# Kernel tuning notes

Hardware: AMD Instinct MI355X
Metric: run time of the kernel (lower is better)

Reference implementation:

```python
import jax, jax.numpy as jnp
import numpy as np


def setup_inputs() -> dict:
    key = jax.random.key(0)
    ks = jax.random.split(key, 8)
    B, IN, H, OUT = 8192, 1024, 2048, 1024
    SIGMA_MIN, SIGMA_MAX, PHASE = 0.9, 0.999, 2.0 * np.pi
    # recurrence decay params, initialized as in the torch module
    rng = np.random.RandomState(0)
    u1 = rng.random_sample(H)
    u2 = rng.random_sample(H)
    v = -0.5 * np.log(u1 * (SIGMA_MAX ** 2 - SIGMA_MIN ** 2) + SIGMA_MIN ** 2)
    theta = u2 * PHASE
    scale_b = 1.0 / np.sqrt(IN)
    scale_c = 1.0 / np.sqrt(H)
    return {
        "x": jax.random.normal(ks[0], (B, IN), dtype=jnp.float32),
        "h_prev": jax.random.normal(ks[1], (B, H), dtype=jnp.float32),
        "Br": jax.random.normal(ks[2], (H, IN), dtype=jnp.float32) * scale_b,
        "Bi": jax.random.normal(ks[3], (H, IN), dtype=jnp.float32) * scale_b,
        "Cr": jax.random.normal(ks[4], (OUT, H), dtype=jnp.float32) * scale_c,
        "Ci": jax.random.normal(ks[5], (OUT, H), dtype=jnp.float32) * scale_c,
        "v_log": jnp.asarray(np.log(v), dtype=jnp.float32),
        "theta_log": jnp.asarray(np.log(theta), dtype=jnp.float32),
    }


def reference(x, h_prev, Br, Bi, Cr, Ci, v_log, theta_log):
    # effective diagonal recurrence weight w = exp(-exp(v_log) + i*exp(theta_log))
    mag = jnp.exp(-jnp.exp(v_log))            # [H]
    ang = jnp.exp(theta_log)                  # [H]
    wr = mag * jnp.cos(ang)
    wi = mag * jnp.sin(ang)
    # h = B(x) + h_prev * w  (h_prev is real -> imag part comes only from wi)
    # complexLinear on real x: real = x@Br^T, imag = x@Bi^T
    hr = jnp.einsum('bi,hi->bh', x, Br) + h_prev * wr   # [B,H]
    hi = jnp.einsum('bi,hi->bh', x, Bi) + h_prev * wi   # [B,H]
    # out = Re(C(h)) = hr@Cr^T - hi@Ci^T
    out = jnp.einsum('bh,oh->bo', hr, Cr) - jnp.einsum('bh,oh->bo', hi, Ci)
    return out
```

## Files before the change

kernel.cpp:

```cpp
#include <hip/hip_runtime.h>
#include <stdint.h>

typedef unsigned short u16;
typedef short bf16x8 __attribute__((ext_vector_type(8)));
typedef float f32x4 __attribute__((ext_vector_type(4)));

typedef void as1_void __attribute__((address_space(1)));
typedef void as3_void __attribute__((address_space(3)));

__device__ inline u16 f32_to_bf16(float f) {
    uint32_t u = __builtin_bit_cast(uint32_t, f);
    u += 0x7fffu + ((u >> 16) & 1u);
    return (u16)(u >> 16);
}

__device__ inline void gld_lds16(const void* g, void* l) {
    __builtin_amdgcn_global_load_lds((as1_void*)g, (as3_void*)l, 16, 0, 0);
}



__global__ void prep_w_kernel(const float* __restrict__ v_log,
                              const float* __restrict__ theta_log,
                              float* __restrict__ wfull, int H) {
    int h = blockIdx.x * blockDim.x + threadIdx.x;
    if (h < H) {
        float mag = expf(-expf(v_log[h]));
        float ang = expf(theta_log[h]);
        wfull[h]     = mag * cosf(ang);
        wfull[h + H] = mag * sinf(ang);
    }
}

__global__ void pack_ccat_kernel(const float* __restrict__ Cr,
                                 const float* __restrict__ Ci,
                                 u16* __restrict__ Ccat, int total4) {
    int i = blockIdx.x * blockDim.x + threadIdx.x;
    if (i >= total4) return;
    int e = i * 4;
    int o = e >> 12;
    int k = e & 4095;
    float4 f; float s;
    if (k < 2048) { f = *(const float4*)(Cr + (size_t)o * 2048 + k);          s =  1.f; }
    else          { f = *(const float4*)(Ci + (size_t)o * 2048 + (k - 2048)); s = -1.f; }
    ushort4 u;
    u.x = f32_to_bf16(s * f.x); u.y = f32_to_bf16(s * f.y);
    u.z = f32_to_bf16(s * f.z); u.w = f32_to_bf16(s * f.w);
    ((ushort4*)Ccat)[i] = u;
}

__global__ void transpose_cast_kernel(const float* __restrict__ Br,
                                      const float* __restrict__ Bi,
                                      u16* __restrict__ Bcat) {
    __shared__ float t[32][33];
    const float* src = blockIdx.z ? Bi : Br;
    int colOff = blockIdx.z ? 2048 : 0;
    int c0 = blockIdx.x * 32, r0 = blockIdx.y * 32;
    int tx = threadIdx.x, ty = threadIdx.y;
#pragma unroll
    for (int j = 0; j < 4; j++)
        t[ty + j * 8][tx] = src[(size_t)(r0 + ty + j * 8) * 1024 + c0 + tx];
    __syncthreads();
#pragma unroll
    for (int j = 0; j < 4; j++)
        Bcat[(size_t)(c0 + ty + j * 8) * 4096 + colOff + r0 + tx] =
            f32_to_bf16(t[tx][ty + j * 8]);
}

__global__ void cast_both_kernel(const float* __restrict__ x,
                                 const float* __restrict__ h_prev,
                                 u16* __restrict__ dst) {
    const int n4x = 8192 * 1024 / 4;
    int i = blockIdx.x * blockDim.x + threadIdx.x;
    float4 f = (i < n4x) ? ((const float4*)x)[i] : ((const float4*)h_prev)[i - n4x];
    ushort4 o;
    o.x = f32_to_bf16(f.x); o.y = f32_to_bf16(f.y);
    o.z = f32_to_bf16(f.z); o.w = f32_to_bf16(f.w);
    ((ushort4*)dst)[i] = o;
}

__global__ void reduce_cw_kernel(const float* __restrict__ partials,
                                 const float* __restrict__ Cr, const float* __restrict__ Ci,
                                 const float* __restrict__ wfull,
                                 u16* __restrict__ Wmain, u16* __restrict__ Cwbf) {
    const int n4_red = 1024 * 1024 / 4;
    const int n4_cw  = 1024 * 2048 / 4;
    int i = blockIdx.x * blockDim.x + threadIdx.x;
    if (i < n4_red) {
        int e = i * 4;
        float4 s = *(const float4*)(partials + e);
#pragma unroll
        for (int z = 1; z < 8; z++) {
            float4 p = *(const float4*)(partials + ((size_t)z << 20) + e);
            s.x += p.x; s.y += p.y; s.z += p.z; s.w += p.w;
        }
        ushort4 u;
        u.x = f32_to_bf16(s.x); u.y = f32_to_bf16(s.y);
        u.z = f32_to_bf16(s.z); u.w = f32_to_bf16(s.w);
        ((ushort4*)Wmain)[i] = u;
    } else if (i < n4_red + n4_cw) {
        int j = i - n4_red;
        int e = j * 4;
        int o = e >> 11;
        int h = e & 2047;
        float4 cr = *(const float4*)(Cr + (size_t)o * 2048 + h);
        float4 ci = *(const float4*)(Ci + (size_t)o * 2048 + h);
        float4 wr = *(const float4*)(wfull + h);
        float4 wi = *(const float4*)(wfull + 2048 + h);
        ushort4 u;
        u.x = f32_to_bf16(cr.x * wr.x - ci.x * wi.x);
        u.y = f32_to_bf16(cr.y * wr.y - ci.y * wi.y);
        u.z = f32_to_bf16(cr.z * wr.z - ci.z * wi.z);
        u.w = f32_to_bf16(cr.w * wr.w - ci.w * wi.w);
        ((ushort4*)Cwbf)[j] = u;
    }
}


__global__ __launch_bounds__(256)
void gemm_splitk_kernel(const u16* __restrict__ A, const u16* __restrict__ B,
                        float* __restrict__ partials)
{
    __shared__ __align__(16) u16 ldsA[128 * 64];
    __shared__ __align__(16) u16 ldsB[128 * 64];
    const int K = 4096;

    const int tid = threadIdx.x, wid = tid >> 6, lane = tid & 63;
    const int quad = lane >> 4, l16 = lane & 15;
    const int wm = wid >> 1, wn = wid & 1;
    const int bm = blockIdx.y, bn = blockIdx.x, bz = blockIdx.z;
    const int kb = bz * 512;

    const u16* gA[4]; const u16* gB[4];
    u16 *lA[4], *lB[4];
#pragma unroll
    for (int t = 0; t < 4; t++) {
        int s = wid * 256 + t * 64 + lane;
        int sr = s >> 3;
        int sj = (s & 7) ^ (sr & 7);
        lA[t] = ldsA + s * 8;
        lB[t] = ldsB + s * 8;
        gA[t] = A + (size_t)(bm * 128 + sr) * K + sj * 8 + kb;
        gB[t] = B + (size_t)(bn * 128 + sr) * K + sj * 8 + kb;
    }

    const f32x4 fz = {0.f, 0.f, 0.f, 0.f};
    f32x4 acc[4][4];
#pragma unroll
    for (int i = 0; i < 4; i++)
#pragma unroll
        for (int j = 0; j < 4; j++) acc[i][j] = fz;

    for (int k0 = 0; k0 < 512; k0 += 64) {
        __syncthreads();
#pragma unroll
        for (int t = 0; t < 4; t++) {
            gld_lds16(gA[t] + k0, lA[t]);
            gld_lds16(gB[t] + k0, lB[t]);
        }
        __syncthreads();
#pragma unroll
        for (int ks = 0; ks < 2; ks++) {
            bf16x8 af[4], bfr[4];
#pragma unroll
            for (int i = 0; i < 4; i++) {
                int r = wm * 64 + i * 16 + l16;
                af[i] = *(const bf16x8*)(ldsA + (r * 8 + ((ks * 4 + quad) ^ (r & 7))) * 8);
            }
#pragma unroll
            for (int j = 0; j < 4; j++) {
                int r = wn * 64 + j * 16 + l16;
                bfr[j] = *(const bf16x8*)(ldsB + (r * 8 + ((ks * 4 + quad) ^ (r & 7))) * 8);
            }
#pragma unroll
            for (int i = 0; i < 4; i++)
#pragma unroll
                for (int j = 0; j < 4; j++)
                    acc[i][j] = __builtin_amdgcn_mfma_f32_16x16x32_bf16(af[i], bfr[j], acc[i][j], 0, 0, 0);
        }
    }

    float* P = partials + ((size_t)bz << 20);
    const int gm = bm * 128 + wm * 64, gn = bn * 128 + wn * 64;
#pragma unroll
    for (int i = 0; i < 4; i++)
#pragma unroll
        for (int j = 0; j < 4; j++) {
            int col = gn + j * 16 + l16;
#pragma unroll
            for (int r = 0; r < 4; r++)
                P[(size_t)(gm + i * 16 + quad * 4 + r) * 1024 + col] = acc[i][j][r];
        }
}


__global__ __launch_bounds__(256)
void gemm_main_kernel(const u16* __restrict__ Axb, const u16* __restrict__ Ahb,
                      const u16* __restrict__ Bw,  const u16* __restrict__ Bcw,
                      float* __restrict__ out)
{
    __shared__ __align__(16) u16 ldsA[128 * 64];
    __shared__ __align__(16) u16 ldsB[128 * 64];

    const int tid = threadIdx.x, wid = tid >> 6, lane = tid & 63;
    const int quad = lane >> 4, l16 = lane & 15;
    const int wm = wid >> 1, wn = wid & 1;
    const int id = blockIdx.x;
    const int bm = id & 63, bn = id >> 6;

    int srow[4], sj[4];
    u16 *lA[4], *lB[4];
#pragma unroll
    for (int t = 0; t < 4; t++) {
        int s = wid * 256 + t * 64 + lane;
        srow[t] = s >> 3;
        sj[t] = (s & 7) ^ (srow[t] & 7);
        lA[t] = ldsA + s * 8;
        lB[t] = ldsB + s * 8;
    }

    const f32x4 fz = {0.f, 0.f, 0.f, 0.f};
    f32x4 acc[4][4];
#pragma unroll
    for (int i = 0; i < 4; i++)
#pragma unroll
        for (int j = 0; j < 4; j++) acc[i][j] = fz;

#pragma unroll 1
    for (int phase = 0; phase < 2; phase++) {
        const u16* Ap = phase ? Ahb : Axb;
        const u16* Bp = phase ? Bcw : Bw;
        const int KS = phase ? 2048 : 1024;
        const u16* gA[4]; const u16* gB[4];
#pragma unroll
        for (int t = 0; t < 4; t++) {
            gA[t] = Ap + (size_t)(bm * 128 + srow[t]) * KS + sj[t] * 8;
            gB[t] = Bp + (size_t)(bn * 128 + srow[t]) * KS + sj[t] * 8;
        }
        for (int k0 = 0; k0 < KS; k0 += 64) {
            __syncthreads();
#pragma unroll
            for (int t = 0; t < 4; t++) {
                gld_lds16(gA[t] + k0, lA[t]);
                gld_lds16(gB[t] + k0, lB[t]);
            }
            __syncthreads();
#pragma unroll
            for (int ks = 0; ks < 2; ks++) {
                bf16x8 af[4], bfr[4];
#pragma unroll
                for (int i = 0; i < 4; i++) {
                    int r = wm * 64 + i * 16 + l16;
                    af[i] = *(const bf16x8*)(ldsA + (r * 8 + ((ks * 4 + quad) ^ (r & 7))) * 8);
                }
#pragma unroll
                for (int j = 0; j < 4; j++) {
                    int r = wn * 64 + j * 16 + l16;
                    bfr[j] = *(const bf16x8*)(ldsB + (r * 8 + ((ks * 4 + quad) ^ (r & 7))) * 8);
                }
#pragma unroll
                for (int i = 0; i < 4; i++)
#pragma unroll
                    for (int j = 0; j < 4; j++)
                        acc[i][j] = __builtin_amdgcn_mfma_f32_16x16x32_bf16(af[i], bfr[j], acc[i][j], 0, 0, 0);
            }
        }
    }

    const int gm = bm * 128 + wm * 64, gn = bn * 128 + wn * 64;
#pragma unroll
    for (int i = 0; i < 4; i++)
#pragma unroll
        for (int j = 0; j < 4; j++) {
            int col = gn + j * 16 + l16;
#pragma unroll
            for (int r = 0; r < 4; r++)
                out[(size_t)(gm + i * 16 + quad * 4 + r) * 1024 + col] = acc[i][j][r];
        }
}


extern "C" void kernel_launch(void* const* d_in, const int* in_sizes, int n_in,
                              void* d_out, int out_size, void* d_ws, size_t ws_size,
                              hipStream_t stream)
{
    const float* x      = (const float*)d_in[0];
    const float* h_prev = (const float*)d_in[1];
    const float* Br     = (const float*)d_in[2];
    const float* Bi     = (const float*)d_in[3];
    const float* Cr     = (const float*)d_in[4];
    const float* Ci     = (const float*)d_in[5];
    const float* v_log  = (const float*)d_in[6];
    const float* th_log = (const float*)d_in[7];
    float* out = (float*)d_out;

    const size_t MB = 1024 * 1024;
    size_t need = 54 * MB + 4096 * 4;
    if (ws_size < need) return;

    char* ws = (char*)d_ws;
    u16*   Ccat     = (u16*)ws;
    u16*   Bcat     = (u16*)(ws + 8 * MB);
    float* partials = (float*)(ws + 16 * MB);
    u16*   x_bf     = (u16*)ws;
    u16*   hp_bf    = (u16*)(ws + 16 * MB);
    u16*   Wmain    = (u16*)(ws + 48 * MB);
    u16*   Cwbf     = (u16*)(ws + 50 * MB);
    float* wfull    = (float*)(ws + 54 * MB);

    prep_w_kernel<<<8, 256, 0, stream>>>(v_log, th_log, wfull, 2048);
    pack_ccat_kernel<<<4096, 256, 0, stream>>>(Cr, Ci, Ccat, 1024 * 4096 / 4);
    transpose_cast_kernel<<<dim3(32, 64, 2), dim3(32, 8), 0, stream>>>(Br, Bi, Bcat);
    gemm_splitk_kernel<<<dim3(8, 8, 8), 256, 0, stream>>>(Ccat, Bcat, partials);
    reduce_cw_kernel<<<3072, 256, 0, stream>>>(partials, Cr, Ci, wfull, Wmain, Cwbf);
    cast_both_kernel<<<24576, 256, 0, stream>>>(x, h_prev, x_bf);
    gemm_main_kernel<<<512, 256, 0, stream>>>(x_bf, hp_bf, Wmain, Cwbf, out);
}
```

Baseline: 250.9 us.

## Fuse prep kernels: merge casts, inline C packing into split-K GEMM, inline w

Merges the x/h_prev cast and the Br/Bi transpose-cast into one launch, removes the separate Ccat packing kernel by having the split-K GEMM load fp32 Cr/Ci and convert them to bf16 (with sign flip) on the fly into LDS, and computes the recurrence weights inline in the reduce kernel instead of a prep kernel. This cuts three kernel launches and one intermediate bf16 buffer round-trip. In exchange, the GEMM A-path now uses register loads instead of async global-to-LDS loads, and the transcendental work is repeated per output row in the reduce kernel. The workspace layout also grows.

Measured after the change: 258.8 us. +3.1%, slower.

```diff
diff --git a/kernel.cpp b/kernel.cpp
--- a/kernel.cpp
+++ b/kernel.cpp
@@ -20,68 +20,44 @@
 
 
 
-__global__ void prep_w_kernel(const float* __restrict__ v_log,
-                              const float* __restrict__ theta_log,
-                              float* __restrict__ wfull, int H) {
-    int h = blockIdx.x * blockDim.x + threadIdx.x;
-    if (h < H) {
-        float mag = expf(-expf(v_log[h]));
-        float ang = expf(theta_log[h]);
-        wfull[h]     = mag * cosf(ang);
-        wfull[h + H] = mag * sinf(ang);
-    }
-}
-
-__global__ void pack_ccat_kernel(const float* __restrict__ Cr,
-                                 const float* __restrict__ Ci,
-                                 u16* __restrict__ Ccat, int total4) {
-    int i = blockIdx.x * blockDim.x + threadIdx.x;
-    if (i >= total4) return;
-    int e = i * 4;
-    int o = e >> 12;
-    int k = e & 4095;
-    float4 f; float s;
-    if (k < 2048) { f = *(const float4*)(Cr + (size_t)o * 2048 + k);          s =  1.f; }
-    else          { f = *(const float4*)(Ci + (size_t)o * 2048 + (k - 2048)); s = -1.f; }
-    ushort4 u;
-    u.x = f32_to_bf16(s * f.x); u.y = f32_to_bf16(s * f.y);
-    u.z = f32_to_bf16(s * f.z); u.w = f32_to_bf16(s * f.w);
-    ((ushort4*)Ccat)[i] = u;
-}
-
-__global__ void transpose_cast_kernel(const float* __restrict__ Br,
-                                      const float* __restrict__ Bi,
-                                      u16* __restrict__ Bcat) {
-    __shared__ float t[32][33];
-    const float* src = blockIdx.z ? Bi : Br;
-    int colOff = blockIdx.z ? 2048 : 0;
-    int c0 = blockIdx.x * 32, r0 = blockIdx.y * 32;
-    int tx = threadIdx.x, ty = threadIdx.y;
-#pragma unroll
-    for (int j = 0; j < 4; j++)
-        t[ty + j * 8][tx] = src[(size_t)(r0 + ty + j * 8) * 1024 + c0 + tx];
-    __syncthreads();
-#pragma unroll
-    for (int j = 0; j < 4; j++)
-        Bcat[(size_t)(c0 + ty + j * 8) * 4096 + colOff + r0 + tx] =
-            f32_to_bf16(t[tx][ty + j * 8]);
-}
-
-__global__ void cast_both_kernel(const float* __restrict__ x,
-                                 const float* __restrict__ h_prev,
-                                 u16* __restrict__ dst) {
+__global__ void bigcast_kernel(const float* __restrict__ x,
+                               const float* __restrict__ h_prev,
+                               const float* __restrict__ Br,
+                               const float* __restrict__ Bi,
+                               u16* __restrict__ xh_bf,
+                               u16* __restrict__ Bcat) {
     const int n4x = 8192 * 1024 / 4;
-    int i = blockIdx.x * blockDim.x + threadIdx.x;
-    float4 f = (i < n4x) ? ((const float4*)x)[i] : ((const float4*)h_prev)[i - n4x];
-    ushort4 o;
-    o.x = f32_to_bf16(f.x); o.y = f32_to_bf16(f.y);
-    o.z = f32_to_bf16(f.z); o.w = f32_to_bf16(f.w);
-    ((ushort4*)dst)[i] = o;
-}
+    const int tid = threadIdx.x;
+    if (blockIdx.x < 24576) {
+        int i = blockIdx.x * 256 + tid;
+        float4 f = (i < n4x) ? ((const float4*)x)[i] : ((const float4*)h_prev)[i - n4x];
+        ushort4 o;
+        o.x = f32_to_bf16(f.x); o.y = f32_to_bf16(f.y);
+        o.z = f32_to_bf16(f.z); o.w = f32_to_bf16(f.w);
+        ((ushort4*)xh_bf)[i] = o;
+    } else {
+        __shared__ float t[32][33];
+        int id2 = blockIdx.x - 24576;
+        const float* src = (id2 >= 2048) ? Bi : Br;
+        int colOff = (id2 >= 2048) ? 2048 : 0;
+        int rem = id2 & 2047;
+        int c0 = (rem & 31) * 32, r0 = (rem >> 5) * 32;
+        int tx = tid & 31, ty = tid >> 5;
+#pragma unroll
+        for (int j = 0; j < 4; j++)
+            t[ty + j * 8][tx] = src[(size_t)(r0 + ty + j * 8) * 1024 + c0 + tx];
+        __syncthreads();
+#pragma unroll
+        for (int j = 0; j < 4; j++)
+            Bcat[(size_t)(c0 + ty + j * 8) * 4096 + colOff + r0 + tx] =
+                f32_to_bf16(t[tx][ty + j * 8]);
+    }
+}
+
 
 __global__ void reduce_cw_kernel(const float* __restrict__ partials,
                                  const float* __restrict__ Cr, const float* __restrict__ Ci,
-                                 const float* __restrict__ wfull,
+                                 const float* __restrict__ v_log, const float* __restrict__ th_log,
                                  u16* __restrict__ Wmain, u16* __restrict__ Cwbf) {
     const int n4_red = 1024 * 1024 / 4;
     const int n4_cw  = 1024 * 2048 / 4;
@@ -105,43 +81,52 @@
         int h = e & 2047;
         float4 cr = *(const float4*)(Cr + (size_t)o * 2048 + h);
         float4 ci = *(const float4*)(Ci + (size_t)o * 2048 + h);
-        float4 wr = *(const float4*)(wfull + h);
-        float4 wi = *(const float4*)(wfull + 2048 + h);
+        float4 vl = *(const float4*)(v_log + h);
+        float4 tl = *(const float4*)(th_log + h);
+        float mag, ang;
         ushort4 u;
-        u.x = f32_to_bf16(cr.x * wr.x - ci.x * wi.x);
-        u.y = f32_to_bf16(cr.y * wr.y - ci.y * wi.y);
-        u.z = f32_to_bf16(cr.z * wr.z - ci.z * wi.z);
-        u.w = f32_to_bf16(cr.w * wr.w - ci.w * wi.w);
+        mag = expf(-expf(vl.x)); ang = expf(tl.x);
+        u.x = f32_to_bf16(cr.x * (mag * cosf(ang)) - ci.x * (mag * sinf(ang)));
+        mag = expf(-expf(vl.y)); ang = expf(tl.y);
+        u.y = f32_to_bf16(cr.y * (mag * cosf(ang)) - ci.y * (mag * sinf(ang)));
+        mag = expf(-expf(vl.z)); ang = expf(tl.z);
+        u.z = f32_to_bf16(cr.z * (mag * cosf(ang)) - ci.z * (mag * sinf(ang)));
+        mag = expf(-expf(vl.w)); ang = expf(tl.w);
+        u.w = f32_to_bf16(cr.w * (mag * cosf(ang)) - ci.w * (mag * sinf(ang)));
         ((ushort4*)Cwbf)[j] = u;
     }
 }
 
 
 __global__ __launch_bounds__(256)
-void gemm_splitk_kernel(const u16* __restrict__ A, const u16* __restrict__ B,
-                        float* __restrict__ partials)
+void gemm_splitk_kernel(const float* __restrict__ Cr, const float* __restrict__ Ci,
+                        const u16* __restrict__ Bcat, float* __restrict__ partials)
 {
     __shared__ __align__(16) u16 ldsA[128 * 64];
     __shared__ __align__(16) u16 ldsB[128 * 64];
-    const int K = 4096;
 
     const int tid = threadIdx.x, wid = tid >> 6, lane = tid & 63;
     const int quad = lane >> 4, l16 = lane & 15;
     const int wm = wid >> 1, wn = wid & 1;
     const int bm = blockIdx.y, bn = blockIdx.x, bz = blockIdx.z;
-    const int kb = bz * 512;
-
-    const u16* gA[4]; const u16* gB[4];
-    u16 *lA[4], *lB[4];
+
+    const float* Asrc = (bz < 4) ? Cr : Ci;
+    const uint32_t sgn_mask = (bz < 4) ? 0u : 0x80000000u;
+    const int akb = (bz < 4) ? bz * 512 : bz * 512 - 2048;
+
+    const int ar = tid >> 1;
+    const int ac = (tid & 1) * 32;
+    const float* agp = Asrc + (size_t)(bm * 128 + ar) * 2048 + akb + ac;
+
+    const u16* gB[4];
+    u16* lB[4];
 #pragma unroll
     for (int t = 0; t < 4; t++) {
         int s = wid * 256 + t * 64 + lane;
         int sr = s >> 3;
         int sj = (s & 7) ^ (sr & 7);
-        lA[t] = ldsA + s * 8;
         lB[t] = ldsB + s * 8;
-        gA[t] = A + (size_t)(bm * 128 + sr) * K + sj * 8 + kb;
-        gB[t] = B + (size_t)(bn * 128 + sr) * K + sj * 8 + kb;
+        gB[t] = Bcat + (size_t)(bn * 128 + sr) * 4096 + sj * 8 + bz * 512;
     }
 
     const f32x4 fz = {0.f, 0.f, 0.f, 0.f};
@@ -154,9 +139,26 @@
     for (int k0 = 0; k0 < 512; k0 += 64) {
         __syncthreads();
 #pragma unroll
-        for (int t = 0; t < 4; t++) {
-            gld_lds16(gA[t] + k0, lA[t]);
+        for (int t = 0; t < 4; t++)
             gld_lds16(gB[t] + k0, lB[t]);
+        float4 av[8];
+#pragma unroll
+        for (int q = 0; q < 8; q++)
+            av[q] = *(const float4*)(agp + k0 + q * 4);
+#pragma unroll
+        for (int c = 0; c < 4; c++) {
+            bf16x8 w;
+            const float4 a0 = av[2 * c], a1 = av[2 * c + 1];
+            w[0] = (short)f32_to_bf16(__builtin_bit_cast(float, __builtin_bit_cast(uint32_t, a0.x) ^ sgn_mask));
+            w[1] = (short)f32_to_bf16(__builtin_bit_cast(float, __builtin_bit_cast(uint32_t, a0.y) ^ sgn_mask));
+            w[2] = (short)f32_to_bf16(__builtin_bit_cast(float, __builtin_bit_cast(uint32_t, a0.z) ^ sgn_mask));
+            w[3] = (short)f32_to_bf16(__builtin_bit_cast(float, __builtin_bit_cast(uint32_t, a0.w) ^ sgn_mask));
+            w[4] = (short)f32_to_bf16(__builtin_bit_cast(float, __builtin_bit_cast(uint32_t, a1.x) ^ sgn_mask));
+            w[5] = (short)f32_to_bf16(__builtin_bit_cast(float, __builtin_bit_cast(uint32_t, a1.y) ^ sgn_mask));
+            w[6] = (short)f32_to_bf16(__builtin_bit_cast(float, __builtin_bit_cast(uint32_t, a1.z) ^ sgn_mask));
+            w[7] = (short)f32_to_bf16(__builtin_bit_cast(float, __builtin_bit_cast(uint32_t, a1.w) ^ sgn_mask));
+            int jg = (ac >> 3) + c;
+            *(bf16x8*)(ldsA + (ar * 8 + (jg ^ (ar & 7))) * 8) = w;
         }
         __syncthreads();
 #pragma unroll
@@ -295,24 +297,20 @@
     float* out = (float*)d_out;
 
     const size_t MB = 1024 * 1024;
-    size_t need = 54 * MB + 4096 * 4;
+    size_t need = 94 * MB;
     if (ws_size < need) return;
 
     char* ws = (char*)d_ws;
-    u16*   Ccat     = (u16*)ws;
-    u16*   Bcat     = (u16*)(ws + 8 * MB);
-    float* partials = (float*)(ws + 16 * MB);
-    u16*   x_bf     = (u16*)ws;
+    u16*   xh_bf    = (u16*)ws;
+    u16*   x_bf     = xh_bf;
     u16*   hp_bf    = (u16*)(ws + 16 * MB);
-    u16*   Wmain    = (u16*)(ws + 48 * MB);
-    u16*   Cwbf     = (u16*)(ws + 50 * MB);
-    float* wfull    = (float*)(ws + 54 * MB);
-
-    prep_w_kernel<<<8, 256, 0, stream>>>(v_log, th_log, wfull, 2048);
-    pack_ccat_kernel<<<4096, 256, 0, stream>>>(Cr, Ci, Ccat, 1024 * 4096 / 4);
-    transpose_cast_kernel<<<dim3(32, 64, 2), dim3(32, 8), 0, stream>>>(Br, Bi, Bcat);
-    gemm_splitk_kernel<<<dim3(8, 8, 8), 256, 0, stream>>>(Ccat, Bcat, partials);
-    reduce_cw_kernel<<<3072, 256, 0, stream>>>(partials, Cr, Ci, wfull, Wmain, Cwbf);
-    cast_both_kernel<<<24576, 256, 0, stream>>>(x, h_prev, x_bf);
+    u16*   Bcat     = (u16*)(ws + 48 * MB);
+    float* partials = (float*)(ws + 56 * MB);
+    u16*   Wmain    = (u16*)(ws + 88 * MB);
+    u16*   Cwbf     = (u16*)(ws + 90 * MB);
+
+    bigcast_kernel<<<28672, 256, 0, stream>>>(x, h_prev, Br, Bi, xh_bf, Bcat);
+    gemm_splitk_kernel<<<dim3(8, 8, 8), 256, 0, stream>>>(Cr, Ci, Bcat, partials);
+    reduce_cw_kernel<<<3072, 256, 0, stream>>>(partials, Cr, Ci, v_log, th_log, Wmain, Cwbf);
     gemm_main_kernel<<<512, 256, 0, stream>>>(x_bf, hp_bf, Wmain, Cwbf, out);
 }
```
